# Performance work log

Hardware: AMD Instinct MI355X
Metric: run time of the kernel (lower is better)

## Reference

```python
import jax, jax.numpy as jnp
import numpy as np

EPS = 1e-07


def setup_inputs() -> dict:
    key = jax.random.key(0)
    k1, k2, k3, k4, k5, k6 = jax.random.split(key, 6)
    B, S, E = 128, 512, 64  # batch, seq_len == n_items, emb_size
    user_emb = jax.random.normal(k1, (B, S, E), dtype=jnp.float32)
    item_emb = jax.random.normal(k2, (B, S, E), dtype=jnp.float32)
    cluster_weights = jax.random.uniform(k3, (B, S, 1), dtype=jnp.float32)
    # binary keep-mask over sequence positions (multiplicative)
    last_item_mask = (jax.random.uniform(k4, (B, 1, S)) > 0.5).astype(jnp.float32)
    proj_w = jax.random.normal(k5, (1, 1), dtype=jnp.float32)
    proj_b = jax.random.normal(k6, (1,), dtype=jnp.float32)
    return {
        "user_emb": user_emb,
        "item_emb": item_emb,
        "cluster_weights": cluster_weights,
        "last_item_mask": last_item_mask,
        "proj_w": proj_w,
        "proj_b": proj_b,
    }


def reference(user_emb, item_emb, cluster_weights, last_item_mask, proj_w, proj_b):
    # L2-normalize with clamped norm (matches torch.clamp(norm, 1e-7))
    u = user_emb / jnp.maximum(jnp.linalg.norm(user_emb, axis=-1, keepdims=True), EPS)
    v = item_emb / jnp.maximum(jnp.linalg.norm(item_emb, axis=-1, keepdims=True), EPS)
    # cosine sim: [B, n_items, seq_len] (n_items == seq_len == S)
    cos = jnp.einsum("bse,bne->bns", u, v)
    # cluster_weights [B,S,1] broadcasts over the seq_len axis, indexed by dim1
    # (faithful to torch broadcast of [B,N,S,1] * [B,S,1,1] with N == S)
    sims = cos * cluster_weights  # [B,N,S]
    # Linear(1,1) + sigmoid applied elementwise (scalar affine)
    sims = jax.nn.sigmoid(sims * proj_w[0, 0] + proj_b[0])
    # permute to [B, seq_len, n_items], mask [B,1,S] broadcasts over last axis
    sims = jnp.swapaxes(sims, 1, 2) * last_item_mask
    # max over dim 2 -> [B, seq_len]
    return jnp.max(sims, axis=2)
```

## Files before the change

### kernel.cpp

```cpp
#include <hip/hip_runtime.h>
#include <hip/hip_bf16.h>
#include <math.h>

#define B_ 128
#define S_ 512
#define E_ 64
#define PAD_ 72

typedef short bf16x8 __attribute__((ext_vector_type(8)));
typedef float f32x4 __attribute__((ext_vector_type(4)));

__device__ __forceinline__ unsigned short f2b(float f) {
  __hip_bfloat16 h = __float2bfloat16(f);
  unsigned short u;
  __builtin_memcpy(&u, &h, 2);
  return u;
}

__device__ __forceinline__ void norm_store(const f32x4 x[4], float scl_num,
                                           unsigned short* dst) {
  float ss = 0.f;
#pragma unroll
  for (int i = 0; i < 4; ++i)
#pragma unroll
    for (int j = 0; j < 4; ++j) ss = fmaf(x[i][j], x[i][j], ss);
  ss += __shfl_xor(ss, 16);
  ss += __shfl_xor(ss, 32);
  float s = scl_num / fmaxf(sqrtf(ss), 1e-7f);
  bf16x8 o0, o1;
#pragma unroll
  for (int i = 0; i < 2; ++i)
#pragma unroll
    for (int j = 0; j < 4; ++j) {
      o0[i * 4 + j] = (short)f2b(x[i][j] * s);
      o1[i * 4 + j] = (short)f2b(x[i + 2][j] * s);
    }
  *(bf16x8*)dst = o0;
  *(bf16x8*)(dst + 8) = o1;
}

__global__ __launch_bounds__(1024) void fused_kernel(
    const float* __restrict__ ue, const float* __restrict__ ve,
    const float* __restrict__ cw, const float* __restrict__ mask,
    const float* __restrict__ pw, const float* __restrict__ pb,
    float* __restrict__ out) {
  __shared__ unsigned short vlds[S_ * PAD_];
  __shared__ unsigned short ulds[256 * PAD_];
  __shared__ float comb[4][256];

  const int bx = blockIdx.x;
  const int b = (bx & 7) * 16 + (bx >> 4);
  const int shalf = (bx >> 3) & 1;

  const int tid = threadIdx.x;
  const int wv = tid >> 6;
  const int lane = tid & 63;
  const int c = lane & 15;
  const int g = lane >> 4;
  const int ws = wv >> 2;
  const int wn = wv & 3;

  const float w0 = pw[0];
  const float* __restrict__ vb = ve + (size_t)b * S_ * E_;
  const float* __restrict__ cwb = cw + (size_t)b * S_;
  const float* __restrict__ ub = ue + ((size_t)b * S_ + shalf * 256) * E_;
  const float* __restrict__ mb = mask + (size_t)b * S_;

  const int vr0 = wv * 32 + c, vr1 = vr0 + 16, ur = wv * 16 + c;
  const f32x4* pv0 = (const f32x4*)(vb + (size_t)vr0 * E_ + g * 16);
  const f32x4* pv1 = (const f32x4*)(vb + (size_t)vr1 * E_ + g * 16);
  const f32x4* pu = (const f32x4*)(ub + (size_t)ur * E_ + g * 16);
  f32x4 xv0[4], xv1[4], xu[4];
#pragma unroll
  for (int i = 0; i < 4; ++i) {
    xv0[i] = pv0[i];
    xv1[i] = pv1[i];
    xu[i] = pu[i];
  }
  float cw0 = cwb[vr0] * w0;
  float cw1 = cwb[vr1] * w0;
  float pen[8];
#pragma unroll
  for (int j = 0; j < 8; ++j)
    pen[j] = (mb[(wn * 8 + j) * 16 + c] > 0.5f) ? 0.0f : -1e30f;

  norm_store(xv0, cw0, vlds + (size_t)vr0 * PAD_ + g * 16);
  norm_store(xv1, cw1, vlds + (size_t)vr1 * PAD_ + g * 16);
  norm_store(xu, 1.0f, ulds + (size_t)ur * PAD_ + g * 16);

  __syncthreads();

  const unsigned short* urp = ulds + (size_t)(ws * 64 + c) * PAD_ + g * 8;
  bf16x8 a[4][2];
#pragma unroll
  for (int st = 0; st < 4; ++st) {
    a[st][0] = *(const bf16x8*)(urp + st * 16 * PAD_);
    a[st][1] = *(const bf16x8*)(urp + st * 16 * PAD_ + 32);
  }

  float r[4][4];
#pragma unroll
  for (int st = 0; st < 4; ++st)
#pragma unroll
    for (int i = 0; i < 4; ++i) r[st][i] = -INFINITY;

#pragma unroll
  for (int j = 0; j < 8; ++j) {
    int it = wn * 8 + j;
    const unsigned short* vr = vlds + (size_t)(it * 16 + c) * PAD_ + g * 8;
    bf16x8 b0 = *(const bf16x8*)(vr);
    bf16x8 b1 = *(const bf16x8*)(vr + 32);
    f32x4 ci = {pen[j], pen[j], pen[j], pen[j]};
#pragma unroll
    for (int st = 0; st < 4; ++st) {
      f32x4 acc = __builtin_amdgcn_mfma_f32_16x16x32_bf16(a[st][0], b0, ci, 0, 0, 0);
      acc = __builtin_amdgcn_mfma_f32_16x16x32_bf16(a[st][1], b1, acc, 0, 0, 0);
      r[st][0] = fmaxf(r[st][0], acc[0]);
      r[st][1] = fmaxf(r[st][1], acc[1]);
      r[st][2] = fmaxf(r[st][2], acc[2]);
      r[st][3] = fmaxf(r[st][3], acc[3]);
    }
  }

#pragma unroll
  for (int st = 0; st < 4; ++st)
#pragma unroll
    for (int i = 0; i < 4; ++i) {
      float v = r[st][i];
      v = fmaxf(v, __shfl_xor(v, 1)); v = fmaxf(v, __shfl_xor(v, 2));
      v = fmaxf(v, __shfl_xor(v, 4)); v = fmaxf(v, __shfl_xor(v, 8));
      r[st][i] = v;
    }

  if (c == 0) {
#pragma unroll
    for (int st = 0; st < 4; ++st)
#pragma unroll
      for (int i = 0; i < 4; ++i)
        comb[wn][ws * 64 + st * 16 + g * 4 + i] = r[st][i];
  }

  __syncthreads();

  if (tid < 256) {
    float v = fmaxf(fmaxf(comb[0][tid], comb[1][tid]),
                    fmaxf(comb[2][tid], comb[3][tid]));
    float bias = pb[0];
    out[(size_t)b * S_ + shalf * 256 + tid] =
        (v < -1e29f) ? 0.0f : 1.0f / (1.0f + expf(-(v + bias)));
  }
}

extern "C" void kernel_launch(void* const* d_in, const int* in_sizes, int n_in,
                              void* d_out, int out_size, void* d_ws, size_t ws_size,
                              hipStream_t stream) {
  const float* ue = (const float*)d_in[0];
  const float* ve = (const float*)d_in[1];
  const float* cw = (const float*)d_in[2];
  const float* mask = (const float*)d_in[3];
  const float* pw = (const float*)d_in[4];
  const float* pb = (const float*)d_in[5];
  float* out = (float*)d_out;

  hipLaunchKernelGGL(fused_kernel, dim3(2 * B_), dim3(1024), 0, stream,
                     ue, ve, cw, mask, pw, pb, out);
}
```

Measured before the change: 19.13 us.

## Coalesce row loads and split item normalization around an extra barrier

Embedding rows are now loaded fully coalesced: each wave reads 16 contiguous rows with lanes striding across them, and norms are reduced with 16-lane shuffles. Normalization of the item rows is split in two. The half matching this block's user half is done before the first barrier, and the other half is done after the A fragments are loaded, followed by a second barrier. This aims to improve global load efficiency and overlap part of the staging work. The cost is one extra block-wide sync and more shuffles per row.

Measured after the change: 19.25 us. Within noise of the previous version (+0.6%).

```diff
diff --git a/kernel.cpp b/kernel.cpp
--- a/kernel.cpp
+++ b/kernel.cpp
@@ -17,26 +17,22 @@
   return u;
 }
 
-__device__ __forceinline__ void norm_store(const f32x4 x[4], float scl_num,
-                                           unsigned short* dst) {
-  float ss = 0.f;
+__device__ __forceinline__ void norm16_proc(const f32x4 x[4],
+                                            const float* __restrict__ sn,
+                                            int c, int g,
+                                            unsigned short* __restrict__ lds_base) {
 #pragma unroll
-  for (int i = 0; i < 4; ++i)
-#pragma unroll
-    for (int j = 0; j < 4; ++j) ss = fmaf(x[i][j], x[i][j], ss);
-  ss += __shfl_xor(ss, 16);
-  ss += __shfl_xor(ss, 32);
-  float s = scl_num / fmaxf(sqrtf(ss), 1e-7f);
-  bf16x8 o0, o1;
-#pragma unroll
-  for (int i = 0; i < 2; ++i)
-#pragma unroll
-    for (int j = 0; j < 4; ++j) {
-      o0[i * 4 + j] = (short)f2b(x[i][j] * s);
-      o1[i * 4 + j] = (short)f2b(x[i + 2][j] * s);
-    }
-  *(bf16x8*)dst = o0;
-  *(bf16x8*)(dst + 8) = o1;
+  for (int i = 0; i < 4; ++i) {
+    float ss = x[i][0] * x[i][0] + x[i][1] * x[i][1] +
+               x[i][2] * x[i][2] + x[i][3] * x[i][3];
+    ss += __shfl_xor(ss, 1); ss += __shfl_xor(ss, 2);
+    ss += __shfl_xor(ss, 4); ss += __shfl_xor(ss, 8);
+    float s = sn[i] / fmaxf(sqrtf(ss), 1e-7f);
+    ushort4 o;
+    o.x = f2b(x[i][0] * s); o.y = f2b(x[i][1] * s);
+    o.z = f2b(x[i][2] * s); o.w = f2b(x[i][3] * s);
+    *(ushort4*)(lds_base + (size_t)(i * 4 + g) * PAD_ + c * 4) = o;
+  }
 }
 
 __global__ __launch_bounds__(1024) void fused_kernel(
@@ -66,27 +62,35 @@
   const float* __restrict__ ub = ue + ((size_t)b * S_ + shalf * 256) * E_;
   const float* __restrict__ mb = mask + (size_t)b * S_;
 
-  const int vr0 = wv * 32 + c, vr1 = vr0 + 16, ur = wv * 16 + c;
-  const f32x4* pv0 = (const f32x4*)(vb + (size_t)vr0 * E_ + g * 16);
-  const f32x4* pv1 = (const f32x4*)(vb + (size_t)vr1 * E_ + g * 16);
-  const f32x4* pu = (const f32x4*)(ub + (size_t)ur * E_ + g * 16);
-  f32x4 xv0[4], xv1[4], xu[4];
+  const int vown = shalf * 256 + wv * 16;
+  const int voth = (1 - shalf) * 256 + wv * 16;
+  const int urow = wv * 16;
+
+  const float* pvo = vb + (size_t)vown * E_;
+  const float* puu = ub + (size_t)urow * E_;
+  const float* pvt = vb + (size_t)voth * E_;
+  f32x4 xvo[4], xu[4], xvt[4];
+#pragma unroll
+  for (int i = 0; i < 4; ++i) xvo[i] = *(const f32x4*)(pvo + i * 256 + lane * 4);
+#pragma unroll
+  for (int i = 0; i < 4; ++i) xu[i] = *(const f32x4*)(puu + i * 256 + lane * 4);
+#pragma unroll
+  for (int i = 0; i < 4; ++i) xvt[i] = *(const f32x4*)(pvt + i * 256 + lane * 4);
+
+  float sno[4], snt[4], snu[4];
 #pragma unroll
   for (int i = 0; i < 4; ++i) {
-    xv0[i] = pv0[i];
-    xv1[i] = pv1[i];
-    xu[i] = pu[i];
+    sno[i] = w0 * cwb[vown + i * 4 + g];
+    snt[i] = w0 * cwb[voth + i * 4 + g];
+    snu[i] = 1.0f;
   }
-  float cw0 = cwb[vr0] * w0;
-  float cw1 = cwb[vr1] * w0;
   float pen[8];
 #pragma unroll
   for (int j = 0; j < 8; ++j)
     pen[j] = (mb[(wn * 8 + j) * 16 + c] > 0.5f) ? 0.0f : -1e30f;
 
-  norm_store(xv0, cw0, vlds + (size_t)vr0 * PAD_ + g * 16);
-  norm_store(xv1, cw1, vlds + (size_t)vr1 * PAD_ + g * 16);
-  norm_store(xu, 1.0f, ulds + (size_t)ur * PAD_ + g * 16);
+  norm16_proc(xvo, sno, c, g, vlds + (size_t)vown * PAD_);
+  norm16_proc(xu, snu, c, g, ulds + (size_t)urow * PAD_);
 
   __syncthreads();
 
@@ -97,6 +101,9 @@
     a[st][0] = *(const bf16x8*)(urp + st * 16 * PAD_);
     a[st][1] = *(const bf16x8*)(urp + st * 16 * PAD_ + 32);
   }
+  norm16_proc(xvt, snt, c, g, vlds + (size_t)voth * PAD_);
+
+  __syncthreads();
 
   float r[4][4];
 #pragma unroll
@@ -106,7 +113,7 @@
 
 #pragma unroll
   for (int j = 0; j < 8; ++j) {
-    int it = wn * 8 + j;
+    const int it = wn * 8 + j;
     const unsigned short* vr = vlds + (size_t)(it * 16 + c) * PAD_ + g * 8;
     bf16x8 b0 = *(const bf16x8*)(vr);
     bf16x8 b1 = *(const bf16x8*)(vr + 32);
```
